# Optimization experiments

Hardware: AMD Instinct MI355X
Metric: run time of the kernel (lower is better)

Reference implementation:

```python
import jax, jax.numpy as jnp
import numpy as np

GROUPS = 8
PAD = 3  # padding = (kernel_size - 1) // 2 with kernel_size = 7


def setup_inputs() -> dict:
    key = jax.random.key(0)
    k0, k1, k2, k3, k4, k5 = jax.random.split(key, 6)
    B, Cin, Cout, H, W, K = 2, 128, 128, 96, 96, 7
    x = jax.random.normal(k0, (B, Cin, H, W), jnp.float32)
    v = jax.random.normal(k1, (B, Cout, H, W), jnp.float32)
    # 1x1 conv weights (kaiming-ish scale), stored as [out, in]
    scale = float(np.sqrt(2.0 / Cout))
    w_q = jax.random.normal(k2, (Cout, Cin), jnp.float32) * scale
    w_k = jax.random.normal(k3, (Cout, Cin), jnp.float32) * scale
    # relative position params: N(0, 1) as in reset_parameters
    rel_h = jax.random.normal(k4, (Cout // 2, 1, 1, K, 1), jnp.float32)
    rel_w = jax.random.normal(k5, (Cout // 2, 1, 1, 1, K), jnp.float32)
    return {"x": x, "v": v, "w_q": w_q, "w_k": w_k, "rel_h": rel_h, "rel_w": rel_w}


def _unfold(t, K, H, W):
    # t: [B, C, H+2P, W+2P] -> [B, C, H, W, K*K] matching torch unfold(2,K,1).unfold(3,K,1) row-major flatten
    return jnp.stack([t[:, :, i:i + H, j:j + W] for i in range(K) for j in range(K)], axis=-1)


def reference(x, v, w_q, w_k, rel_h, rel_w):
    B, Cin, H, W = x.shape
    K = rel_h.shape[3]
    Cout = w_q.shape[0]
    G = GROUPS
    P = PAD

    # 1x1 convs (bias=False); pad-then-conv == conv-then-pad for zero pad, no bias
    q = jnp.einsum('bihw,oi->bohw', x, w_q)            # [B, Cout, H, W]
    kf = jnp.einsum('bihw,oi->bohw', x, w_k)           # [B, Cout, H, W]

    kpad = jnp.pad(kf, ((0, 0), (0, 0), (P, P), (P, P)))
    vpad = jnp.pad(v, ((0, 0), (0, 0), (P, P), (P, P)))

    kk = _unfold(kpad, K, H, W).reshape(B, Cout, H, W, K, K)   # [B,C,H,W,kh,kw]
    vv = _unfold(vpad, K, H, W)                                 # [B,C,H,W,K*K]

    C2 = Cout // 2
    kk = jnp.concatenate([kk[:, :C2] + rel_h, kk[:, C2:] + rel_w], axis=1)
    kk = kk.reshape(B, G, Cout // G, H, W, K * K)
    vv = vv.reshape(B, G, Cout // G, H, W, K * K)
    qq = q.reshape(B, G, Cout // G, H, W, 1)

    attn = jax.nn.softmax(qq * kk, axis=-1)            # per-channel softmax over k*k window
    out = jnp.einsum('bgchwk,bgchwk->bgchw', attn, vv)
    return out.reshape(B, Cout, H, W)
```

## Files before the change

kernel.cpp:

```cpp
#include <hip/hip_runtime.h>
#include <hip/hip_bf16.h>

#define HW 9216
#define CIN 128
#define COUT 128

typedef _Float16 half8 __attribute__((ext_vector_type(8)));
typedef float f32x4 __attribute__((ext_vector_type(4)));

__device__ __forceinline__ float fast_exp2(float x) {
    float r;
    asm("v_exp_f32 %0, %1" : "=v"(r) : "v"(x));
    return r;
}

__device__ __forceinline__ void mfma16(f32x4& d, half8 a, half8 b) {
    asm("v_mfma_f32_16x16x32_f16 %0, %1, %2, %0" : "+v"(d) : "v"(a), "v"(b));
}

__device__ __forceinline__ void gl_lds16(const void* g, void* l) {
    __builtin_amdgcn_global_load_lds(
        (const __attribute__((address_space(1))) unsigned int*)g,
        (__attribute__((address_space(3))) unsigned int*)l, 16, 0, 0);
}

__device__ __forceinline__ unsigned short h_bits(_Float16 h) {
    return __builtin_bit_cast(unsigned short, h);
}

__global__ __launch_bounds__(256) void prep(
    const float* __restrict__ x,
    const float* __restrict__ wq, const float* __restrict__ wk,
    _Float16* __restrict__ xh_t, _Float16* __restrict__ xl_t,
    _Float16* __restrict__ wh_t, _Float16* __restrict__ wl_t)
{
    const int tid = threadIdx.x;
    const int bx = blockIdx.x;
    const int b = blockIdx.y;

    if (bx >= 144) {
        if (b) return;
        int o = (bx - 144) * 32 + (tid >> 3);
        int k0 = (tid & 7) * 16;
        const float* src = (o < 128) ? (wq + o * 128) : (wk + (o - 128) * 128);
        float vals[16];
        #pragma unroll
        for (int t = 0; t < 4; ++t)
            *(float4*)&vals[t * 4] = *(const float4*)&src[k0 + t * 4];
        half8 h0, h1, l0, l1;
        #pragma unroll
        for (int j = 0; j < 8; ++j) {
            _Float16 h = (_Float16)vals[j];
            h0[j] = h; l0[j] = (_Float16)(vals[j] - (float)h);
            _Float16 h2 = (_Float16)vals[j + 8];
            h1[j] = h2; l1[j] = (_Float16)(vals[j + 8] - (float)h2);
        }
        int s = (o & 7) << 3;
        *(half8*)&wh_t[o * 128 + (k0 ^ s)]       = h0;
        *(half8*)&wh_t[o * 128 + ((k0 + 8) ^ s)] = h1;
        *(half8*)&wl_t[o * 128 + (k0 ^ s)]       = l0;
        *(half8*)&wl_t[o * 128 + ((k0 + 8) ^ s)] = l1;
        return;
    }

    __shared__ unsigned int lds[64 * 128];
    const int pixbase = bx * 64;
    const int p = tid & 63;
    const int kw = tid >> 6;
    const float* xb = x + (size_t)b * CIN * HW + pixbase + p;

    #pragma unroll
    for (int i = 0; i < 32; ++i) {
        int k = kw * 32 + i;
        float v = xb[(size_t)k * HW];
        _Float16 h = (_Float16)v;
        _Float16 l = (_Float16)(v - (float)h);
        unsigned int pack = (unsigned int)h_bits(h) | ((unsigned int)h_bits(l) << 16);
        lds[(p * 128 + k) ^ (p & 31)] = pack;
    }
    __syncthreads();

    const int p2 = tid >> 2;
    const int qk = (tid & 3) * 32;
    const int s = (p2 & 7) << 3;
    unsigned int hw_[16], lw_[16];
    #pragma unroll
    for (int i = 0; i < 16; ++i) {
        int pos0 = qk + 2 * i;
        int src0 = pos0 ^ s;
        unsigned int a0 = lds[(p2 * 128 + src0) ^ (p2 & 31)];
        unsigned int a1 = lds[(p2 * 128 + src0 + 1) ^ (p2 & 31)];
        hw_[i] = (a0 & 0xffffu) | (a1 << 16);
        lw_[i] = (a0 >> 16) | (a1 & 0xffff0000u);
    }
    size_t orow = ((size_t)b * HW + pixbase + p2) * 64 + (qk >> 1);
    unsigned int* oh = (unsigned int*)xh_t;
    unsigned int* ol = (unsigned int*)xl_t;
    #pragma unroll
    for (int i = 0; i < 4; ++i) {
        uint4 th = {hw_[i*4], hw_[i*4+1], hw_[i*4+2], hw_[i*4+3]};
        uint4 tl = {lw_[i*4], lw_[i*4+1], lw_[i*4+2], lw_[i*4+3]};
        *(uint4*)&oh[orow + i * 4] = th;
        *(uint4*)&ol[orow + i * 4] = tl;
    }
}

__global__ __launch_bounds__(256) void conv_mfma(
    const _Float16* __restrict__ xh_t, const _Float16* __restrict__ xl_t,
    const _Float16* __restrict__ wh_t, const _Float16* __restrict__ wl_t,
    float* __restrict__ qbuf, float* __restrict__ kbuf)
{
    __shared__ _Float16 xsh[128 * 64];
    __shared__ _Float16 xsl[128 * 64];
    __shared__ _Float16 wsh[128 * 64];
    __shared__ _Float16 wsl[128 * 64];

    const int tid = threadIdx.x;
    const int lane = tid & 63;
    const int wave = tid >> 6;
    const int pixbase = blockIdx.x * 128;
    const int b = blockIdx.y;
    const int half = blockIdx.z;
    const int wbase = half * 128;

    const int wrow = (wave & 1) * 64;
    const int wpix = (wave >> 1) * 64;

    f32x4 acc[4][4];
    #pragma unroll
    for (int m = 0; m < 4; ++m)
        #pragma unroll
        for (int n = 0; n < 4; ++n) { acc[m][n][0]=0.f; acc[m][n][1]=0.f; acc[m][n][2]=0.f; acc[m][n][3]=0.f; }

    const size_t xrow = ((size_t)b * HW + pixbase) * 128;

    #pragma unroll
    for (int kc = 0; kc < 2; ++kc) {
        if (kc) __syncthreads();
        #pragma unroll
        for (int i = 0; i < 4; ++i) {
            int sgl = wave * 4 + i;
            int pix = sgl * 8 + (lane >> 3);
            int j = lane & 7;
            const _Float16* gh = xh_t + xrow + (size_t)pix * 128 + kc * 64 + j * 8;
            const _Float16* gl = xl_t + xrow + (size_t)pix * 128 + kc * 64 + j * 8;
            gl_lds16(gh, (void*)(xsh + sgl * 512));
            gl_lds16(gl, (void*)(xsl + sgl * 512));
        }
        #pragma unroll
        for (int i = 0; i < 4; ++i) {
            int sgl = wave * 4 + i;
            int o = sgl * 8 + (lane >> 3);
            int j = lane & 7;
            const _Float16* gh = wh_t + (size_t)(wbase + o) * 128 + kc * 64 + j * 8;
            const _Float16* gl = wl_t + (size_t)(wbase + o) * 128 + kc * 64 + j * 8;
            gl_lds16(gh, (void*)(wsh + sgl * 512));
            gl_lds16(gl, (void*)(wsl + sgl * 512));
        }
        __syncthreads();

        #pragma unroll
        for (int ks = 0; ks < 2; ++ks) {
            const int kb = ks * 32 + (lane >> 4) * 8;
            half8 ah[4], al[4];
            #pragma unroll
            for (int m = 0; m < 4; ++m) {
                int o = wrow + m * 16 + (lane & 15);
                int idx = (o * 64 + kb) ^ ((o & 7) << 3);
                ah[m] = *(const half8*)&wsh[idx];
                al[m] = *(const half8*)&wsl[idx];
            }
            #pragma unroll
            for (int n = 0; n < 4; ++n) {
                int p = wpix + n * 16 + (lane & 15);
                int idx = (p * 64 + kb) ^ ((p & 7) << 3);
                half8 bh = *(const half8*)&xsh[idx];
                half8 bl = *(const half8*)&xsl[idx];
                #pragma unroll
                for (int m = 0; m < 4; ++m) {
                    mfma16(acc[m][n], ah[m], bh);
                    mfma16(acc[m][n], al[m], bh);
                    mfma16(acc[m][n], ah[m], bl);
                }
            }
        }
    }

    asm volatile("s_nop 7\n\ts_nop 7"
        : "+v"(acc[0][0]), "+v"(acc[0][1]), "+v"(acc[0][2]), "+v"(acc[0][3]),
          "+v"(acc[1][0]), "+v"(acc[1][1]), "+v"(acc[1][2]), "+v"(acc[1][3]),
          "+v"(acc[2][0]), "+v"(acc[2][1]), "+v"(acc[2][2]), "+v"(acc[2][3]),
          "+v"(acc[3][0]), "+v"(acc[3][1]), "+v"(acc[3][2]), "+v"(acc[3][3]));

    float* obuf = half ? kbuf : qbuf;
    #pragma unroll
    for (int m = 0; m < 4; ++m) {
        #pragma unroll
        for (int n = 0; n < 4; ++n) {
            int pc = pixbase + wpix + n * 16 + (lane & 15);
            #pragma unroll
            for (int r = 0; r < 4; ++r) {
                int row = wrow + m * 16 + (lane >> 4) * 4 + r;
                obuf[((size_t)b * COUT + row) * HW + pc] = acc[m][n][r];
            }
        }
    }
}

__global__ __launch_bounds__(128, 6) void attn_v9(
    const float* __restrict__ qbuf,
    const float* __restrict__ kbuf,
    const float* __restrict__ v,
    const float* __restrict__ rel_h,
    const float* __restrict__ rel_w,
    float* __restrict__ out)
{
    __shared__ __align__(16) float ks[22 * 40];
    __shared__ __align__(16) float vs[22 * 40];

    const int tid = threadIdx.x;
    const int tile = blockIdx.x;
    const int bc = blockIdx.y;
    const int c = bc & 127;
    const int th = (tile / 3) * 16;
    const int tw = (tile % 3) * 32;

    const float* kp = kbuf + (size_t)bc * HW;
    const float* vp = v    + (size_t)bc * HW;

    for (int idx = tid; idx < 22 * 38; idx += 128) {
        int r = idx / 38, cl = idx - r * 38;
        int gr = th - 3 + r, gc = tw - 3 + cl;
        bool ok = ((unsigned)gr < 96u) && ((unsigned)gc < 96u);
        ks[r * 40 + cl] = ok ? kp[gr * 96 + gc] : 0.f;
        vs[r * 40 + cl] = ok ? vp[gr * 96 + gc] : 0.f;
    }

    const bool is_h = (c < 64);
    const float* rbase = is_h ? (rel_h + c * 7) : (rel_w + (c - 64) * 7);
    float r7[7];
    #pragma unroll
    for (int i = 0; i < 7; ++i) r7[i] = rbase[i];

    const int ty = tid >> 3;
    const int tx = tid & 7;

    const float* qrow = qbuf + (size_t)bc * HW + (th + ty) * 96 + tw + tx * 4;
    float4 qa = *(const float4*)qrow;
    const float L2E = 1.4426950408889634f;
    float q2[4] = {qa.x * L2E, qa.y * L2E, qa.z * L2E, qa.w * L2E};

    float s[4] = {0.f, 0.f, 0.f, 0.f};
    float a[4] = {0.f, 0.f, 0.f, 0.f};

    __syncthreads();

    const float* kb0 = &ks[ty * 40 + tx * 4];
    const float* vb0 = &vs[ty * 40 + tx * 4];

    #pragma unroll
    for (int dh = 0; dh < 7; ++dh) {
        float kr[12], vr[12];
        #pragma unroll
        for (int t = 0; t < 3; ++t) {
            *(float4*)&kr[t * 4] = *(const float4*)&kb0[dh * 40 + t * 4];
            *(float4*)&vr[t * 4] = *(const float4*)&vb0[dh * 40 + t * 4];
        }

        if (is_h) {
            float rh = r7[dh];
            #pragma unroll
            for (int j = 0; j < 4; ++j) {
                float qr = q2[j] * rh;
                #pragma unroll
                for (int dw = 0; dw < 7; ++dw) {
                    float e = fast_exp2(fmaf(q2[j], kr[j + dw], qr));
                    s[j] += e;
                    a[j] = fmaf(e, vr[j + dw], a[j]);
                }
            }
        } else {
            #pragma unroll
            for (int j = 0; j < 4; ++j) {
                #pragma unroll
                for (int dw = 0; dw < 7; ++dw) {
                    float e = fast_exp2(q2[j] * (kr[j + dw] + r7[dw]));
                    s[j] += e;
                    a[j] = fmaf(e, vr[j + dw], a[j]);
                }
            }
        }
    }

    float* orow = out + (size_t)bc * HW + (th + ty) * 96 + tw + tx * 4;
    float4 o4;
    o4.x = a[0] * __builtin_amdgcn_rcpf(s[0]);
    o4.y = a[1] * __builtin_amdgcn_rcpf(s[1]);
    o4.z = a[2] * __builtin_amdgcn_rcpf(s[2]);
    o4.w = a[3] * __builtin_amdgcn_rcpf(s[3]);
    *(float4*)orow = o4;
}

extern "C" void kernel_launch(void* const* d_in, const int* in_sizes, int n_in,
                              void* d_out, int out_size, void* d_ws, size_t ws_size,
                              hipStream_t stream) {
    const float* x  = (const float*)d_in[0];
    const float* v  = (const float*)d_in[1];
    const float* wq = (const float*)d_in[2];
    const float* wk = (const float*)d_in[3];
    const float* rh = (const float*)d_in[4];
    const float* rw = (const float*)d_in[5];
    float* out = (float*)d_out;

    float* qbuf = (float*)d_ws;
    float* kbuf = qbuf + (size_t)2 * COUT * HW;
    _Float16* xh = (_Float16*)(kbuf + (size_t)2 * COUT * HW);
    _Float16* xl = xh + (size_t)2 * HW * 128;
    _Float16* wh = xl + (size_t)2 * HW * 128;
    _Float16* wl = wh + 256 * 128;

    prep<<<dim3(152, 2), 256, 0, stream>>>(x, wq, wk, xh, xl, wh, wl);
    conv_mfma<<<dim3(72, 2, 2), 256, 0, stream>>>(xh, xl, wh, wl, qbuf, kbuf);
    attn_v9<<<dim3(18, 256), 128, 0, stream>>>(qbuf, kbuf, v, rh, rw, out);
}
```

Before: 50.38 us.

## Make attention kernel persistent with double-buffered LDS and register-prefetched tiles

The attention kernel becomes persistent: 1024 blocks of 256 threads loop over 2304 tiles of 32x32 pixels. The next tile's k/v halo and q values are prefetched into registers while the current tile is computed, then written into an alternate LDS buffer. The larger tiles cut halo overhead per pixel, and the prefetch is meant to hide global load latency behind the exp-heavy compute. In exchange there is more register and LDS pressure, and load imbalance because tiles do not divide evenly across blocks.

Result: faster. 48.35 us (median of 2 runs) (-4.0%).

```diff
diff --git a/kernel.cpp b/kernel.cpp
--- a/kernel.cpp
+++ b/kernel.cpp
@@ -4,6 +4,8 @@
 #define HW 9216
 #define CIN 128
 #define COUT 128
+#define NTILES 2304
+#define NBLK 1024
 
 typedef _Float16 half8 __attribute__((ext_vector_type(8)));
 typedef float f32x4 __attribute__((ext_vector_type(4)));
@@ -207,7 +209,7 @@
     }
 }
 
-__global__ __launch_bounds__(128, 6) void attn_v9(
+__global__ __launch_bounds__(256) void attn_v11(
     const float* __restrict__ qbuf,
     const float* __restrict__ kbuf,
     const float* __restrict__ v,
@@ -215,90 +217,129 @@
     const float* __restrict__ rel_w,
     float* __restrict__ out)
 {
-    __shared__ __align__(16) float ks[22 * 40];
-    __shared__ __align__(16) float vs[22 * 40];
+    __shared__ __align__(16) float ks[2][38 * 40];
+    __shared__ __align__(16) float vs[2][38 * 40];
 
     const int tid = threadIdx.x;
-    const int tile = blockIdx.x;
-    const int bc = blockIdx.y;
-    const int c = bc & 127;
-    const int th = (tile / 3) * 16;
-    const int tw = (tile % 3) * 32;
-
-    const float* kp = kbuf + (size_t)bc * HW;
-    const float* vp = v    + (size_t)bc * HW;
-
-    for (int idx = tid; idx < 22 * 38; idx += 128) {
-        int r = idx / 38, cl = idx - r * 38;
-        int gr = th - 3 + r, gc = tw - 3 + cl;
-        bool ok = ((unsigned)gr < 96u) && ((unsigned)gc < 96u);
-        ks[r * 40 + cl] = ok ? kp[gr * 96 + gc] : 0.f;
-        vs[r * 40 + cl] = ok ? vp[gr * 96 + gc] : 0.f;
-    }
-
-    const bool is_h = (c < 64);
-    const float* rbase = is_h ? (rel_h + c * 7) : (rel_w + (c - 64) * 7);
-    float r7[7];
-    #pragma unroll
-    for (int i = 0; i < 7; ++i) r7[i] = rbase[i];
-
     const int ty = tid >> 3;
     const int tx = tid & 7;
-
-    const float* qrow = qbuf + (size_t)bc * HW + (th + ty) * 96 + tw + tx * 4;
-    float4 qa = *(const float4*)qrow;
     const float L2E = 1.4426950408889634f;
-    float q2[4] = {qa.x * L2E, qa.y * L2E, qa.z * L2E, qa.w * L2E};
-
-    float s[4] = {0.f, 0.f, 0.f, 0.f};
-    float a[4] = {0.f, 0.f, 0.f, 0.f};
-
-    __syncthreads();
-
-    const float* kb0 = &ks[ty * 40 + tx * 4];
-    const float* vb0 = &vs[ty * 40 + tx * 4];
-
-    #pragma unroll
-    for (int dh = 0; dh < 7; ++dh) {
-        float kr[12], vr[12];
-        #pragma unroll
-        for (int t = 0; t < 3; ++t) {
-            *(float4*)&kr[t * 4] = *(const float4*)&kb0[dh * 40 + t * 4];
-            *(float4*)&vr[t * 4] = *(const float4*)&vb0[dh * 40 + t * 4];
-        }
-
-        if (is_h) {
-            float rh = r7[dh];
-            #pragma unroll
-            for (int j = 0; j < 4; ++j) {
-                float qr = q2[j] * rh;
+
+    float kstg[6], vstg[6];
+    float4 qstg;
+
+    int t = blockIdx.x;
+
+    {
+        int bc = t / 9, tl = t - bc * 9;
+        int th = (tl / 3) * 32, tw = (tl % 3) * 32;
+        const float* kp = kbuf + (size_t)bc * HW;
+        const float* vp = v    + (size_t)bc * HW;
+        #pragma unroll
+        for (int i = 0; i < 6; ++i) {
+            int idx = tid + i * 256;
+            int r = idx / 38, cl = idx - r * 38;
+            int gr = th - 3 + r, gc = tw - 3 + cl;
+            bool ok = (idx < 1444) && ((unsigned)gr < 96u) && ((unsigned)gc < 96u);
+            kstg[i] = ok ? kp[gr * 96 + gc] : 0.f;
+            vstg[i] = ok ? vp[gr * 96 + gc] : 0.f;
+        }
+        qstg = *(const float4*)(qbuf + (size_t)bc * HW + (th + ty) * 96 + tw + tx * 4);
+    }
+
+    int cur = 0;
+    for (;;) {
+        const int bc = t / 9, tl = t - bc * 9;
+        const int th = (tl / 3) * 32, tw = (tl % 3) * 32;
+        const int c = bc & 127;
+        const bool is_h = (c < 64);
+        const float* rbase = is_h ? (rel_h + c * 7) : (rel_w + (c - 64) * 7);
+        float r7[7];
+        #pragma unroll
+        for (int i = 0; i < 7; ++i) r7[i] = rbase[i];
+        float q2[4] = {qstg.x * L2E, qstg.y * L2E, qstg.z * L2E, qstg.w * L2E};
+
+        #pragma unroll
+        for (int i = 0; i < 6; ++i) {
+            int idx = tid + i * 256;
+            if (idx < 1444) {
+                int r = idx / 38, cl = idx - r * 38;
+                ks[cur][r * 40 + cl] = kstg[i];
+                vs[cur][r * 40 + cl] = vstg[i];
+            }
+        }
+        __syncthreads();
+
+        const int tn = t + NBLK;
+        const bool more = (tn < NTILES);
+        if (more) {
+            int bc2 = tn / 9, tl2 = tn - bc2 * 9;
+            int th2 = (tl2 / 3) * 32, tw2 = (tl2 % 3) * 32;
+            const float* kp = kbuf + (size_t)bc2 * HW;
+            const float* vp = v    + (size_t)bc2 * HW;
+            #pragma unroll
+            for (int i = 0; i < 6; ++i) {
+                int idx = tid + i * 256;
+                int r = idx / 38, cl = idx - r * 38;
+                int gr = th2 - 3 + r, gc = tw2 - 3 + cl;
+                bool ok = (idx < 1444) && ((unsigned)gr < 96u) && ((unsigned)gc < 96u);
+                kstg[i] = ok ? kp[gr * 96 + gc] : 0.f;
+                vstg[i] = ok ? vp[gr * 96 + gc] : 0.f;
+            }
+            qstg = *(const float4*)(qbuf + (size_t)bc2 * HW + (th2 + ty) * 96 + tw2 + tx * 4);
+        }
+
+        float s[4] = {0.f, 0.f, 0.f, 0.f};
+        float a[4] = {0.f, 0.f, 0.f, 0.f};
+        const float* kb0 = &ks[cur][ty * 40 + tx * 4];
+        const float* vb0 = &vs[cur][ty * 40 + tx * 4];
+
+        #pragma unroll
+        for (int dh = 0; dh < 7; ++dh) {
+            float kr[12], vr[12];
+            #pragma unroll
+            for (int tt = 0; tt < 3; ++tt) {
+                *(float4*)&kr[tt * 4] = *(const float4*)&kb0[dh * 40 + tt * 4];
+                *(float4*)&vr[tt * 4] = *(const float4*)&vb0[dh * 40 + tt * 4];
+            }
+
+            if (is_h) {
+                float rh = r7[dh];
                 #pragma unroll
-                for (int dw = 0; dw < 7; ++dw) {
-                    float e = fast_exp2(fmaf(q2[j], kr[j + dw], qr));
-                    s[j] += e;
-                    a[j] = fmaf(e, vr[j + dw], a[j]);
+                for (int j = 0; j < 4; ++j) {
+                    float qr = q2[j] * rh;
+                    #pragma unroll
+                    for (int dw = 0; dw < 7; ++dw) {
+                        float e = fast_exp2(fmaf(q2[j], kr[j + dw], qr));
+                        s[j] += e;
+                        a[j] = fmaf(e, vr[j + dw], a[j]);
+                    }
                 }
-            }
-        } else {
-            #pragma unroll
-            for (int j = 0; j < 4; ++j) {
+            } else {
                 #pragma unroll
-                for (int dw = 0; dw < 7; ++dw) {
-                    float e = fast_exp2(q2[j] * (kr[j + dw] + r7[dw]));
-                    s[j] += e;
-                    a[j] = fmaf(e, vr[j + dw], a[j]);
+                for (int j = 0; j < 4; ++j) {
+                    #pragma unroll
+                    for (int dw = 0; dw < 7; ++dw) {
+                        float e = fast_exp2(q2[j] * (kr[j + dw] + r7[dw]));
+                        s[j] += e;
+                        a[j] = fmaf(e, vr[j + dw], a[j]);
+                    }
                 }
             }
         }
-    }
-
-    float* orow = out + (size_t)bc * HW + (th + ty) * 96 + tw + tx * 4;
-    float4 o4;
-    o4.x = a[0] * __builtin_amdgcn_rcpf(s[0]);
-    o4.y = a[1] * __builtin_amdgcn_rcpf(s[1]);
-    o4.z = a[2] * __builtin_amdgcn_rcpf(s[2]);
-    o4.w = a[3] * __builtin_amdgcn_rcpf(s[3]);
-    *(float4*)orow = o4;
+
+        float* orow = out + (size_t)bc * HW + (th + ty) * 96 + tw + tx * 4;
+        float4 o4;
+        o4.x = a[0] * __builtin_amdgcn_rcpf(s[0]);
+        o4.y = a[1] * __builtin_amdgcn_rcpf(s[1]);
+        o4.z = a[2] * __builtin_amdgcn_rcpf(s[2]);
+        o4.w = a[3] * __builtin_amdgcn_rcpf(s[3]);
+        *(float4*)orow = o4;
+
+        if (!more) break;
+        t = tn;
+        cur ^= 1;
+    }
 }
 
 extern "C" void kernel_launch(void* const* d_in, const int* in_sizes, int n_in,
@@ -321,5 +362,5 @@
 
     prep<<<dim3(152, 2), 256, 0, stream>>>(x, wq, wk, xh, xl, wh, wl);
     conv_mfma<<<dim3(72, 2, 2), 256, 0, stream>>>(xh, xl, wh, wl, qbuf, kbuf);
-    attn_v9<<<dim3(18, 256), 128, 0, stream>>>(qbuf, kbuf, v, rh, rw, out);
-}
+    attn_v11<<<dim3(NBLK), 256, 0, stream>>>(qbuf, kbuf, v, rh, rw, out);
+}
```
